# Performance work log

Measured on AMD Instinct MI355X. Metric: run time of the kernel, lower is better.

The kernel has to match this reference:

```python
import jax, jax.numpy as jnp
import numpy as np

B, S, T, E, H, V = 32, 64, 64, 512, 512, 32000  # batch, src len, tgt len, embed, hidden(per dir), vocab


def _lstm_scan(xs, Wih, Whh, bih, bhh, h0, c0):
    # xs: [S, B, E]; PyTorch gate order i, f, g, o
    def step(carry, x):
        h, c = carry
        g = x @ Wih.T + bih + h @ Whh.T + bhh
        i, f, gg, o = jnp.split(g, 4, axis=-1)
        c = jax.nn.sigmoid(f) * c + jax.nn.sigmoid(i) * jnp.tanh(gg)
        h = jax.nn.sigmoid(o) * jnp.tanh(c)
        return (h, c), h
    (hT, cT), hs = jax.lax.scan(step, (h0, c0), xs)
    return hs, hT, cT


def setup_inputs() -> dict:
    key = jax.random.key(0)
    ks = jax.random.split(key, 20)
    p = lambda k, shape, s=0.05: (jax.random.normal(k, shape, jnp.float32) * s)
    inp = {
        "input_chunk": jax.random.randint(ks[0], (B, S), 0, V),
        "target_chunk": jax.random.randint(ks[1], (B, T), 0, V),
        "enc_emb": jax.random.uniform(ks[2], (V, E), jnp.float32, -0.1, 0.1),
        "dec_emb": jax.random.uniform(ks[3], (V, E), jnp.float32, -0.1, 0.1),
        # encoder bidirectional LSTM (1 layer)
        "Wih_f": p(ks[4], (4 * H, E)), "Whh_f": p(ks[5], (4 * H, H)),
        "bih_f": p(ks[6], (4 * H,)), "bhh_f": p(ks[7], (4 * H,)),
        "Wih_b": p(ks[8], (4 * H, E)), "Whh_b": p(ks[9], (4 * H, H)),
        "bih_b": p(ks[10], (4 * H,)), "bhh_b": p(ks[11], (4 * H,)),
        # decoder LSTMCell: input 2H+E, hidden 2H
        "Wih_d": p(ks[12], (8 * H, 2 * H + E)), "Whh_d": p(ks[13], (8 * H, 2 * H)),
        "bih_d": p(ks[14], (8 * H,)), "bhh_d": p(ks[15], (8 * H,)),
        # attention projection 2H -> 2H
        "Wa": p(ks[16], (2 * H, 2 * H)), "ba": p(ks[17], (2 * H,)),
        # output projection 2H -> V (bias initialized to 0 in the module)
        "Wout": p(ks[18], (V, 2 * H)), "bout": jnp.zeros((V,), jnp.float32),
    }
    return inp


def reference(input_chunk, target_chunk, enc_emb, dec_emb,
              Wih_f, Whh_f, bih_f, bhh_f, Wih_b, Whh_b, bih_b, bhh_b,
              Wih_d, Whh_d, bih_d, bhh_d, Wa, ba, Wout, bout):
    # ---- Encoder: bidirectional LSTM ----
    x = enc_emb[input_chunk]                 # [B, S, E]
    xs = jnp.transpose(x, (1, 0, 2))         # [S, B, E]
    h0 = jnp.zeros((B, H), x.dtype)
    c0 = jnp.zeros((B, H), x.dtype)
    hs_f, hT_f, cT_f = _lstm_scan(xs, Wih_f, Whh_f, bih_f, bhh_f, h0, c0)
    hs_b, hT_b, cT_b = _lstm_scan(xs[::-1], Wih_b, Whh_b, bih_b, bhh_b, h0, c0)
    hs_b = hs_b[::-1]
    all_hidden = jnp.concatenate([hs_f, hs_b], axis=-1)          # [S, B, 2H]
    all_hidden = jnp.transpose(all_hidden, (1, 0, 2))            # [B, S, 2H]
    dec_h = jnp.concatenate([hT_f, hT_b], axis=-1)               # [B, 2H]
    dec_c = jnp.concatenate([cT_f, cT_b], axis=-1)               # [B, 2H]

    # ---- Decoder: attention + LSTMCell loop (teacher forcing = 1.0, no dropout) ----
    A = all_hidden @ Wa.T + ba               # W_attention(all_hidden), constant across steps
    tgt_emb = dec_emb[target_chunk]          # [B, T, E]
    # feed at t=0 is zeros; afterwards the t-th target embedding
    feeds = jnp.concatenate([jnp.zeros((B, 1, E), tgt_emb.dtype), tgt_emb[:, :-1]], axis=1)
    feeds = jnp.transpose(feeds, (1, 0, 2))  # [T, B, E]

    def dstep(carry, feed):
        h, c = carry
        scores = jnp.einsum('bsd,bd->bs', A, h)                  # [B, S]
        attn = jax.nn.softmax(scores, axis=1)
        ctx = jnp.einsum('bs,bsd->bd', attn, all_hidden)         # [B, 2H]
        inp = jnp.concatenate([ctx, feed], axis=1)               # [B, 2H+E]
        g = inp @ Wih_d.T + bih_d + h @ Whh_d.T + bhh_d
        i, f, gg, o = jnp.split(g, 4, axis=-1)
        c = jax.nn.sigmoid(f) * c + jax.nn.sigmoid(i) * jnp.tanh(gg)
        h = jax.nn.sigmoid(o) * jnp.tanh(c)
        logits = h @ Wout.T + bout                               # [B, V]
        return (h, c), logits

    _, logits = jax.lax.scan(dstep, (dec_h, dec_c), feeds)       # [T, B, V]
    logits = jnp.transpose(logits, (1, 0, 2))                    # [B, T, V]
    outputs = jnp.argmax(logits, axis=-1)                        # [B, T]
    return logits, outputs
```

## Files before the change

### kernel.cpp

```cpp
#include <hip/hip_runtime.h>
#include <hip/hip_bf16.h>

#define BB 32
#define SS 64
#define TT 64
#define EE 512
#define HH 512
#define VV 32000

#define O_C0    0u
#define O_C1    32768u
#define O_HD    65536u
#define O_CD    98304u
#define O_PENC  131072u
#define O_PDEC  655360u
#define O_CTX   1179648u
#define O_ALLH  1212416u
#define O_AATT  3309568u
#define O_HDEC  5406720u
#define O_PACK  7503872u
#define O_DA1   7507968u
#define O_DA2   7540736u
#define O_W1    7573504u
#define WS_NEED 95830016ull

#define S_GXF   0u
#define S_GXB   4194304u
#define S_GFEED 8388608u
#define U_BASE  17000000u

typedef float f32x4 __attribute__((ext_vector_type(4)));
typedef _Float16 f16x8 __attribute__((ext_vector_type(8)));
typedef _Float16 f16x4 __attribute__((ext_vector_type(4)));

__device__ __forceinline__ float sigm_(float x){ return 1.0f/(1.0f + expf(-x)); }

__device__ __forceinline__ unsigned int fkey_(float f){
  unsigned int u = __float_as_uint(f);
  return (u & 0x80000000u) ? ~u : (u | 0x80000000u);
}

__device__ __forceinline__ int swz_(int row, int kb){
  return (row*64 + kb) ^ ((row & 7) << 4);
}

__global__ __launch_bounds__(256) void k_init(float* __restrict__ ws){
  int i = blockIdx.x*256 + threadIdx.x;
  if (i < 65536) ws[i] = 0.0f;
  if (i < 2048) ((unsigned long long*)(ws + O_PACK))[i] = 0ull;
}

__global__ __launch_bounds__(256) void k_cvtW(
    const float* __restrict__ Whh_f, const float* __restrict__ Whh_b,
    const float* __restrict__ Wih_d, const float* __restrict__ Whh_d,
    _Float16* __restrict__ dst)
{
  int g = blockIdx.x*256 + threadIdx.x;
  int idx = g*4;
  f32x4 v;
  if (idx < 1048576){
    v = *(const f32x4*)(Whh_f + idx);
  } else if (idx < 2097152){
    v = *(const f32x4*)(Whh_b + (idx - 1048576));
  } else {
    int j = idx - 2097152;
    int row = j >> 11, col = j & 2047;
    const float* src = (col < 1024) ? (Wih_d + (size_t)row*1536 + col)
                                    : (Whh_d + (size_t)row*1024 + (col - 1024));
    v = *(const f32x4*)src;
  }
  f16x4 h;
  #pragma unroll
  for (int c = 0; c < 4; ++c) h[c] = (_Float16)v[c];
  *(f16x4*)(dst + idx) = h;
}

__global__ __launch_bounds__(256) void k_cvtWout(
    const float* __restrict__ Wout, _Float16* __restrict__ W1)
{
  size_t i = ((size_t)blockIdx.x*256 + threadIdx.x)*8;
  f32x4 x0 = *(const f32x4*)(Wout + i);
  f32x4 x1 = *(const f32x4*)(Wout + i + 4);
// ... 47 lines not shown
    Bs[(kq*4+3)*68 + lrow] = vw.w;
    __syncthreads();
    #pragma unroll
    for (int kk = 0; kk < 16; ++kk){
      float4 a4 = *(const float4*)&As[kk*68 + ty*4];
      float4 b4 = *(const float4*)&Bs[kk*68 + tx*4];
      float av[4] = {a4.x,a4.y,a4.z,a4.w};
      float bv[4] = {b4.x,b4.y,b4.z,b4.w};
      #pragma unroll
      for (int i=0;i<4;++i)
        #pragma unroll
        for (int j=0;j<4;++j)
          acc[i][j] = fmaf(av[i], bv[j], acc[i][j]);
    }
    __syncthreads();
  }
  float bv[4];
  #pragma unroll
  for (int j = 0; j < 4; ++j){
    int n = n0 + tx*4 + j;
    float bb = 0.f;
    if (bias0) bb += bias0[n];
    if (bias1) bb += bias1[n];
    bv[j] = bb;
  }
  #pragma unroll
  for (int i = 0; i < 4; ++i){
    int m = m0 + ty*4 + i;
    float4 v = make_float4(acc[i][0]+bv[0], acc[i][1]+bv[1], acc[i][2]+bv[2], acc[i][3]+bv[3]);
    *(float4*)&C[(size_t)m*ldC + n0 + tx*4] = v;
  }
}

__global__ __launch_bounds__(256) void k_enc_step(
    const _Float16* __restrict__ wenc,
    float* __restrict__ ws, const float* __restrict__ oscr, int t)
{
  __shared__ float hl[128*36];
  __shared__ float Wt[32*132];
  int sub = blockIdx.x, kp = blockIdx.y, dir = blockIdx.z;
  int tid = threadIdx.x;
  int s = dir ? (63 - t) : t;
  int p = t & 1;
  const float* gx  = oscr + (dir ? S_GXB : S_GXF);
  const float* prd = ws + (p ? O_PDEC : O_PENC) + dir*262144u;
  const float* cin = ws + O_C0 + p*32768u + dir*16384u;
  float* cout = ws + O_C0 + (p^1)*32768u + dir*16384u;

  {
    int ug = tid & 31, bg = tid >> 5;
    int ul0 = ug*4;
    int u0 = kp*128 + ul0;
    #pragma unroll
    for (int j = 0; j < 4; ++j){
      int b = bg*4 + j;
      size_t gbase = (size_t)(s*32 + b)*2048u;
      f32x4 g0 = *(const f32x4*)&gx[gbase + u0];
      f32x4 g1 = *(const f32x4*)&gx[gbase + 512 + u0];
      f32x4 g2 = *(const f32x4*)&gx[gbase + 1024 + u0];
      f32x4 g3 = *(const f32x4*)&gx[gbase + 1536 + u0];
      if (t > 0){
        #pragma unroll
        for (int kq = 0; kq < 4; ++kq){
          const float* pp = prd + kq*65536u + (size_t)b*2048u;
          g0 += *(const f32x4*)&pp[u0];
          g1 += *(const f32x4*)&pp[512 + u0];
          g2 += *(const f32x4*)&pp[1024 + u0];
          g3 += *(const f32x4*)&pp[1536 + u0];
        }
      }
      f32x4 c = *(const f32x4*)&cin[b*512 + u0];
      f32x4 cn, hn;
      #pragma unroll
      for (int e = 0; e < 4; ++e){
        float cc = sigm_(g1[e])*c[e] + sigm_(g0[e])*tanhf(g2[e]);
        float hh = sigm_(g3[e])*tanhf(cc);
        cn[e] = cc; hn[e] = hh;
        hl[(ul0+e)*36 + b] = hh;
      }
      if (sub == 0){
        *(f32x4*)&cout[b*512 + u0] = cn;
        *(f32x4*)&ws[O_ALLH + (size_t)(b*64 + s)*1024u + dir*512 + u0] = hn;
      }
    }
  }
  __syncthreads();
  if (t == 63) return;

  const _Float16* W = wenc + dir*1048576u;
  float* P = ws + (p ? O_PENC : O_PDEC) + dir*262144u + kp*65536u;
  int rg2 = tid & 31, bg2 = tid >> 5;
  int wrow = tid & 127, whalf = tid >> 7;
  float acc[4][4] = {};
  for (int kt = 0; kt < 4; ++kt){
    #pragma unroll
    for (int i = 0; i < 4; ++i){
      int chunk = whalf*4 + i;
      int grow = sub*128 + wrow;
      f16x4 v = *(const f16x4*)&W[(size_t)grow*512 + kp*128 + kt*32 + chunk*4];
      Wt[(chunk*4+0)*132 + wrow] = (float)v[0];
      Wt[(chunk*4+1)*132 + wrow] = (float)v[1];
      Wt[(chunk*4+2)*132 + wrow] = (float)v[2];
      Wt[(chunk*4+3)*132 + wrow] = (float)v[3];
    }
    __syncthreads();
    #pragma unroll 8
    for (int kk = 0; kk < 32; ++kk){
      f32x4 wv = *(const f32x4*)&Wt[kk*132 + rg2*4];
      f32x4 hv = *(const f32x4*)&hl[(kt*32+kk)*36 + bg2*4];
      #pragma unroll
      for (int i = 0; i < 4; ++i)
        #pragma unroll
        for (int j = 0; j < 4; ++j)
          acc[i][j] = fmaf(wv[i], hv[j], acc[i][j]);
    }
    __syncthreads();
  }
  #pragma unroll
  for (int j = 0; j < 4; ++j){
    int b = bg2*4 + j;
    f32x4 v; v[0]=acc[0][j]; v[1]=acc[1][j]; v[2]=acc[2][j]; v[3]=acc[3][j];
    *(f32x4*)&P[(size_t)b*2048u + sub*128 + rg2*4] = v;
  }
}

__global__ __launch_bounds__(256) void k_concat(float* __restrict__ ws){
  int i = blockIdx.x*256 + threadIdx.x;
  int which = i >> 15;
  int idx = i & 32767;
  int b = idx >> 10, u = idx & 1023;
  int dir = (u >= 512);
  int uu = u & 511;
  float v;
  if (which == 0){
    int s = dir ? 0 : 63;
    v = ws[O_ALLH + (size_t)(b*64 + s)*1024u + u];
  } else {
    v = ws[O_C0 + dir*16384u + b*512 + uu];
  }
  ws[(which ? O_CD : O_HD) + b*1024 + u] = v;
}

__global__ __launch_bounds__(256) void k_dec_gemm(
    const _Float16* __restrict__ wdec, float* __restrict__ ws)
{
  __shared__ char lds[16384];
  int nb = blockIdx.x, kp = blockIdx.y;
  int tid = threadIdx.x;
  int lane = tid & 63, w = tid >> 6;
  int lr = lane & 15, lg = lane >> 4;
  const _Float16* A1g = (const _Float16*)(ws + O_DA1);
  const _Float16* A2g = (const _Float16*)(ws + O_DA2);

  int aslot = tid & 127;
  int isA2  = tid >> 7;
  int arow = aslot >> 2, aseg = aslot & 3;
  int wrow = tid >> 2, wseg = tid & 3;
  const _Float16* asrc = (isA2 ? A2g : A1g) + (size_t)arow*2048u + kp*512 + aseg*8;
  const _Float16* wsrc = wdec + (size_t)(nb*64 + wrow)*2048u + kp*512 + wseg*8;

  f32x4 accH[2], accM[2];
  #pragma unroll
  for (int i = 0; i < 2; ++i){ f32x4 z; z[0]=z[1]=z[2]=z[3]=0.f; accH[i]=z; accM[i]=z; }

  uint4 rA, rW;
  rA = *(const uint4*)(asrc);
  rW = *(const uint4*)(wsrc);

  for (int kt = 0; kt < 16; ++kt){
    int cur = kt & 1;
    char* base = lds + cur*8192;
    *(uint4*)(base + (isA2 ? 2048 : 0) + swz_(arow, aseg*16)) = rA;
    *(uint4*)(base + 4096 + swz_(wrow, wseg*16)) = rW;
    __syncthreads();
    if (kt < 15){
      rA = *(const uint4*)(asrc + (kt+1)*32);
      rW = *(const uint4*)(wsrc + (kt+1)*32);
    }
    char* A1t = base, *A2t = base + 2048, *Wt = base + 4096;
    f16x8 wf = *(const f16x8*)(Wt + swz_(w*16 + lr, lg*16));
    #pragma unroll
    for (int mf = 0; mf < 2; ++mf){
      f16x8 a1 = *(const f16x8*)(A1t + swz_(mf*16 + lr, lg*16));
      f16x8 a2 = *(const f16x8*)(A2t + swz_(mf*16 + lr, lg*16));
      accH[mf] = __builtin_amdgcn_mfma_f32_16x16x32_f16(a1, wf, accH[mf], 0, 0, 0);
      accM[mf] = __builtin_amdgcn_mfma_f32_16x16x32_f16(a2, wf, accM[mf], 0, 0, 0);
    }
    __syncthreads();
  }
  const float rs = 1.0f/2048.0f;
  float* P = ws + O_PDEC + (size_t)kp*131072u;
  #pragma unroll
  for (int mf = 0; mf < 2; ++mf)
    #pragma unroll
    for (int r = 0; r < 4; ++r){
      int b = mf*16 + lg*4 + r;
      int n = nb*64 + w*16 + lr;
      P[(size_t)b*4096u + n] = accH[mf][r] + accM[mf][r]*rs;
    }
}

__global__ __launch_bounds__(256) void k_attn(float* __restrict__ ws,
                                              const float* __restrict__ oscr, int t){
  __shared__ float hlq[1024];
  __shared__ float part[64][5];
  __shared__ float sc[64];
  __shared__ float atn[64];
  __shared__ float dsh;
  int b = blockIdx.x, tid = threadIdx.x;
  float* hd = ws + O_HD;
  float* cd = ws + O_CD;
  _Float16* DA1 = (_Float16*)(ws + O_DA1);
  _Float16* DA2 = (_Float16*)(ws + O_DA2);
  if (t > 0){
    const float* gfd = oscr + S_GFEED + (size_t)((t-1)*32 + b)*4096u;
    const float* pd = ws + O_PDEC;
    for (int u = tid; u < 1024; u += 256){
      float g0 = gfd[u], g1 = gfd[1024+u], g2 = gfd[2048+u], g3 = gfd[3072+u];
      #pragma unroll
      for (int kp = 0; kp < 4; ++kp){
        const float* p = pd + (size_t)kp*131072u + (size_t)b*4096u;
        g0 += p[u]; g1 += p[1024+u]; g2 += p[2048+u]; g3 += p[3072+u];
      }
      float c = cd[b*1024 + u];
      c = sigm_(g1)*c + sigm_(g0)*tanhf(g2);
      float h = sigm_(g3)*tanhf(c);
      cd[b*1024+u] = c; hd[b*1024+u] = h; hlq[u] = h;
      ws[O_HDEC + (size_t)(b*64 + (t-1))*1024u + u] = h;
      _Float16 hi = (_Float16)h;
      DA1[(size_t)b*2048u + 1024 + u] = hi;
      DA2[(size_t)b*2048u + 1024 + u] = (_Float16)((h - (float)hi)*2048.0f);
    }
  } else {
    for (int u = tid; u < 1024; u += 256){
      float h = hd[b*1024 + u];
      hlq[u] = h;
      _Float16 hi = (_Float16)h;
      DA1[(size_t)b*2048u + 1024 + u] = hi;
      DA2[(size_t)b*2048u + 1024 + u] = (_Float16)((h - (float)hi)*2048.0f);
    }
  }
  __syncthreads();
  {
    int s = tid >> 2, p = tid & 3;
    const float* Ar = ws + O_AATT + (size_t)(b*64 + s)*1024u + p*256;
    const float* hp = &hlq[p*256];
    float sum = 0.f;
    #pragma unroll 8
    for (int k4 = 0; k4 < 64; ++k4){
      float4 a = *(const float4*)&Ar[k4*4];
      float4 h4 = *(const float4*)&hp[k4*4];
      sum = fmaf(a.x,h4.x, fmaf(a.y,h4.y, fmaf(a.z,h4.z, fmaf(a.w,h4.w, sum))));
    }
    part[s][p] = sum;
  }
  __syncthreads();
  if (tid < 64) sc[tid] = part[tid][0] + part[tid][1] + part[tid][2] + part[tid][3];
  __syncthreads();
  if (tid < 64){
    float m = sc[0];
    #pragma unroll
    for (int i = 1; i < 64; ++i) m = fmaxf(m, sc[i]);
    atn[tid] = expf(sc[tid] - m);
  }
  __syncthreads();
  if (tid == 0){
    float d = 0.f;
    #pragma unroll
    for (int i = 0; i < 64; ++i) d += atn[i];
    dsh = 1.0f/d;
  }
  __syncthreads();
  {
    float rd = dsh;
    float ax=0.f, ay=0.f, az=0.f, aw=0.f;
    const float* ah = ws + O_ALLH + (size_t)(b*64)*1024u + tid*4;
    for (int s2 = 0; s2 < 64; ++s2){
      float a = atn[s2];
      float4 v = *(const float4*)&ah[(size_t)s2*1024u];
      ax = fmaf(a, v.x, ax); ay = fmaf(a, v.y, ay);
      az = fmaf(a, v.z, az); aw = fmaf(a, v.w, aw);
    }
    float o[4] = {ax*rd, ay*rd, az*rd, aw*rd};
    #pragma unroll
    for (int j = 0; j < 4; ++j){
      int u = tid*4 + j;
      _Float16 hi = (_Float16)o[j];
      DA1[(size_t)b*2048u + u] = hi;
      DA2[(size_t)b*2048u + u] = (_Float16)((o[j] - (float)hi)*2048.0f);
    }
  }
}

__global__ __launch_bounds__(256) void k_dec_pw_last(float* __restrict__ ws,
                                                     const float* __restrict__ oscr){
  int g = blockIdx.x*256 + threadIdx.x;
  int b = g >> 10, u = g & 1023;
  const float* gfd = oscr + S_GFEED + (size_t)(63*32 + b)*4096u;
  const float* pd = ws + O_PDEC;
  float g0 = gfd[u], g1 = gfd[1024+u], g2 = gfd[2048+u], g3 = gfd[3072+u];
  #pragma unroll
  for (int kp = 0; kp < 4; ++kp){
    const float* p = pd + (size_t)kp*131072u + (size_t)b*4096u;
    g0 += p[u]; g1 += p[1024+u]; g2 += p[2048+u]; g3 += p[3072+u];
  }
  float c = ws[O_CD + b*1024 + u];
  c = sigm_(g1)*c + sigm_(g0)*tanhf(g2);
  float h = sigm_(g3)*tanhf(c);
  ws[O_HDEC + (size_t)(b*64 + 63)*1024u + u] = h;
}

__global__ __launch_bounds__(256) void k_cvtA(float* __restrict__ ws){
  const float* src = ws + O_HDEC;
  _Float16* A1 = (_Float16*)(ws + O_ALLH);
  _Float16* A2 = (_Float16*)(ws + O_AATT);
  int i = (blockIdx.x*256 + threadIdx.x)*8;
  f32x4 x0 = *(const f32x4*)&src[i];
  f32x4 x1 = *(const f32x4*)&src[i+4];
  f16x4 h0, h1, l0, l1;
  #pragma unroll
  for (int c = 0; c < 4; ++c){
    _Float16 a = (_Float16)x0[c];
    h0[c] = a; l0[c] = (_Float16)((x0[c] - (float)a)*2048.0f);
    _Float16 bq = (_Float16)x1[c];
    h1[c] = bq; l1[c] = (_Float16)((x1[c] - (float)bq)*2048.0f);
  }
  *(f16x4*)&A1[i]   = h0;
  *(f16x4*)&A1[i+4] = h1;
  *(f16x4*)&A2[i]   = l0;
  *(f16x4*)&A2[i+4] = l1;
}

__global__ __launch_bounds__(256) void k_logits(
    const _Float16* __restrict__ A1, const _Float16* __restrict__ A2,
    const _Float16* __restrict__ W1, const float* __restrict__ bout,
    float* __restrict__ out, unsigned long long* __restrict__ pk)
{
  __shared__ char lds[49152];
  int tid = threadIdx.x;
  int n0 = blockIdx.x*128, m0 = blockIdx.y*128;
  int lane = tid & 63, wave = tid >> 6;
  int wm = wave >> 1, wn = wave & 1;
  int lr = lane & 15, lg = lane >> 4;

  int s0 = tid*2, s1 = tid*2 + 1;
  int ar0 = s0 >> 2, as0 = s0 & 3;
  int ar1 = s1 >> 2, as1 = s1 & 3;
  const _Float16* a1p0 = A1 + (size_t)(m0 + ar0)*1024u + as0*8;
  const _Float16* a1p1 = A1 + (size_t)(m0 + ar1)*1024u + as1*8;
  const _Float16* a2p0 = A2 + (size_t)(m0 + ar0)*1024u + as0*8;
  const _Float16* a2p1 = A2 + (size_t)(m0 + ar1)*1024u + as1*8;
  const _Float16* wp0  = W1 + (size_t)(n0 + ar0)*1024u + as0*8;
  const _Float16* wp1  = W1 + (size_t)(n0 + ar1)*1024u + as1*8;

  f32x4 accH[4][4], accM[4][4];
  #pragma unroll
  for (int i = 0; i < 4; ++i)
    #pragma unroll
    for (int j = 0; j < 4; ++j){
      f32x4 z; z[0]=z[1]=z[2]=z[3]=0.f;
      accH[i][j] = z; accM[i][j] = z;
    }

  uint4 r10, r11, r20, r21, rw0, rw1;
  r10 = *(const uint4*)a1p0; r11 = *(const uint4*)a1p1;
  r20 = *(const uint4*)a2p0; r21 = *(const uint4*)a2p1;
  rw0 = *(const uint4*)wp0;  rw1 = *(const uint4*)wp1;

  for (int kt = 0; kt < 32; ++kt){
    int cur = kt & 1;
    char* base = lds + cur*24576;
    char* A1t = base, *A2t = base + 8192, *Wt = base + 16384;
    *(uint4*)(A1t + swz_(ar0, as0*16)) = r10;
// ... 184 lines not shown
  const float* enc_emb = (const float*)d_in[2];
  const float* dec_emb = (const float*)d_in[3];
  const float* Wih_f = (const float*)d_in[4];
  const float* Whh_f = (const float*)d_in[5];
  const float* bih_f = (const float*)d_in[6];
  const float* bhh_f = (const float*)d_in[7];
  const float* Wih_b = (const float*)d_in[8];
  const float* Whh_b = (const float*)d_in[9];
  const float* bih_b = (const float*)d_in[10];
  const float* bhh_b = (const float*)d_in[11];
  const float* Wih_d = (const float*)d_in[12];
  const float* Whh_d = (const float*)d_in[13];
  const float* bih_d = (const float*)d_in[14];
  const float* bhh_d = (const float*)d_in[15];
  const float* Wa   = (const float*)d_in[16];
  const float* ba   = (const float*)d_in[17];
  const float* Wout = (const float*)d_in[18];
  const float* bout = (const float*)d_in[19];
  float* ws = (float*)d_ws;
  float* out = (float*)d_out;
  float* oscr = (float*)d_out;
  _Float16* wf16 = (_Float16*)(oscr + U_BASE);
  bool bigws = (ws_size >= WS_NEED);

  k_init<<<256, 256, 0, stream>>>(ws);
  k_cvtW<<<10240, 256, 0, stream>>>(Whh_f, Whh_b, Wih_d, Whh_d, wf16);
  if (bigws)
    k_cvtWout<<<16000, 256, 0, stream>>>(Wout, (_Float16*)(ws + O_W1));

  k_gemm<1><<<dim3(32,32), 256, 0, stream>>>(enc_emb, 512, input_chunk, Wih_f, 512, bih_f, bhh_f, oscr + S_GXF, 2048, 512);
  k_gemm<1><<<dim3(32,32), 256, 0, stream>>>(enc_emb, 512, input_chunk, Wih_b, 512, bih_b, bhh_b, oscr + S_GXB, 2048, 512);
  k_gemm<2><<<dim3(64,32), 256, 0, stream>>>(dec_emb, 512, target_chunk, Wih_d + 1024, 1536, bih_d, bhh_d, oscr + S_GFEED, 4096, 512);

  for (int t = 0; t < 64; ++t){
    k_enc_step<<<dim3(16,4,2), 256, 0, stream>>>(wf16, ws, oscr, t);
  }

  k_concat<<<256, 256, 0, stream>>>(ws);
  k_gemm<0><<<dim3(16,32), 256, 0, stream>>>(ws + O_ALLH, 1024, nullptr, Wa, 1024, ba, nullptr, ws + O_AATT, 1024, 1024);

  const _Float16* wdec = wf16 + 2097152u;
  for (int t = 0; t < 64; ++t){
    k_attn<<<32, 256, 0, stream>>>(ws, oscr, t);
    k_dec_gemm<<<dim3(64,4), 256, 0, stream>>>(wdec, ws);
  }
  k_dec_pw_last<<<128, 256, 0, stream>>>(ws, oscr);

  k_cvtA<<<1024, 256, 0, stream>>>(ws);
  if (bigws){
    k_logits<<<dim3(250,16), 256, 0, stream>>>(
        (const _Float16*)(ws + O_ALLH), (const _Float16*)(ws + O_AATT),
        (const _Float16*)(ws + O_W1), bout, out, (unsigned long long*)(ws + O_PACK));
  } else {
    k_logits_fb<<<dim3(125,4), 512, 0, stream>>>(
        (const _Float16*)(ws + O_ALLH), (const _Float16*)(ws + O_AATT),
        Wout, bout, out, (unsigned long long*)(ws + O_PACK));
  }
  k_argmax<<<8, 256, 0, stream>>>((const unsigned long long*)(ws + O_PACK), out);
}
```

Baseline: 3.565 ms.

## Fuse per-step encoder and decoder launches into persistent kernels with grid barriers

Replaces the 64 per-timestep encoder launches and the 128 decoder attention/GEMM launches with two persistent kernels. Steps are synchronised by an atomic grid-wide barrier in workspace memory, and the concat, last-step pointwise and conversion kernels are folded in. The aim is to remove kernel launch overhead and inter-kernel gaps on the serial recurrence. The barrier assumes all blocks are co-resident and adds spin-wait cost per step. The logits grid is also reordered so that M tiles vary fastest.

```diff
diff --git a/kernel.cpp b/kernel.cpp
--- a/kernel.cpp
+++ b/kernel.cpp
@@ -44,10 +44,21 @@
   return (row*64 + kb) ^ ((row & 7) << 4);
 }
 
+__device__ __forceinline__ void gbar_(unsigned int* bar, unsigned int target){
+  __syncthreads();
+  if (threadIdx.x == 0){
+    __hip_atomic_fetch_add(bar, 1u, __ATOMIC_RELEASE, __HIP_MEMORY_SCOPE_AGENT);
+    while (__hip_atomic_load(bar, __ATOMIC_ACQUIRE, __HIP_MEMORY_SCOPE_AGENT) < target)
+      __builtin_amdgcn_s_sleep(2);
+  }
+  __syncthreads();
+}
+
 __global__ __launch_bounds__(256) void k_init(float* __restrict__ ws){
   int i = blockIdx.x*256 + threadIdx.x;
   if (i < 65536) ws[i] = 0.0f;
   if (i < 2048) ((unsigned long long*)(ws + O_PACK))[i] = 0ull;
+  if (i < 4) ((unsigned int*)(ws + O_CTX))[i] = 0u;
 }
 
 __global__ __launch_bounds__(256) void k_cvtW(
@@ -161,303 +172,318 @@
   }
 }
 
-__global__ __launch_bounds__(256) void k_enc_step(
+__global__ __launch_bounds__(256) void k_enc_all(
     const _Float16* __restrict__ wenc,
-    float* __restrict__ ws, const float* __restrict__ oscr, int t)
+    float* __restrict__ ws, const float* __restrict__ oscr)
 {
   __shared__ float hl[128*36];
   __shared__ float Wt[32*132];
-  int sub = blockIdx.x, kp = blockIdx.y, dir = blockIdx.z;
+  int bid = blockIdx.x;
+  int sub = bid & 15, kp = (bid >> 4) & 3, dir = bid >> 6;
   int tid = threadIdx.x;
-  int s = dir ? (63 - t) : t;
-  int p = t & 1;
-  const float* gx  = oscr + (dir ? S_GXB : S_GXF);
-  const float* prd = ws + (p ? O_PDEC : O_PENC) + dir*262144u;
-  const float* cin = ws + O_C0 + p*32768u + dir*16384u;
-  float* cout = ws + O_C0 + (p^1)*32768u + dir*16384u;
-
-  {
-    int ug = tid & 31, bg = tid >> 5;
-    int ul0 = ug*4;
-    int u0 = kp*128 + ul0;
+  unsigned int* bar = (unsigned int*)(ws + O_CTX);
+  const float* gx = oscr + (dir ? S_GXB : S_GXF);
+  const _Float16* W = wenc + dir*1048576u;
+
+  for (int t = 0; t < 64; ++t){
+    int s = dir ? (63 - t) : t;
+    int p = t & 1;
+    const float* prd = ws + (p ? O_PDEC : O_PENC) + dir*262144u;
+    const float* cin = ws + O_C0 + p*32768u + dir*16384u;
+    float* cout = ws + O_C0 + (p^1)*32768u + dir*16384u;
+
+    {
+      int ug = tid & 31, bg = tid >> 5;
+      int ul0 = ug*4;
+      int u0 = kp*128 + ul0;
+      #pragma unroll
+      for (int j = 0; j < 4; ++j){
+        int b = bg*4 + j;
+        size_t gbase = (size_t)(s*32 + b)*2048u;
+        f32x4 g0 = *(const f32x4*)&gx[gbase + u0];
+        f32x4 g1 = *(const f32x4*)&gx[gbase + 512 + u0];
+        f32x4 g2 = *(const f32x4*)&gx[gbase + 1024 + u0];
+        f32x4 g3 = *(const f32x4*)&gx[gbase + 1536 + u0];
+        if (t > 0){
+          #pragma unroll
+          for (int kq = 0; kq < 4; ++kq){
+            const float* pp = prd + kq*65536u + (size_t)b*2048u;
+            g0 += *(const f32x4*)&pp[u0];
+            g1 += *(const f32x4*)&pp[512 + u0];
+            g2 += *(const f32x4*)&pp[1024 + u0];
+            g3 += *(const f32x4*)&pp[1536 + u0];
+          }
+        }
+        f32x4 c = *(const f32x4*)&cin[b*512 + u0];
+        f32x4 cn, hn;
+        #pragma unroll
+        for (int e = 0; e < 4; ++e){
+          float cc = sigm_(g1[e])*c[e] + sigm_(g0[e])*tanhf(g2[e]);
+          float hh = sigm_(g3[e])*tanhf(cc);
+          cn[e] = cc; hn[e] = hh;
+          hl[(ul0+e)*36 + b] = hh;
+        }
+        if (sub == 0){
+          *(f32x4*)&cout[b*512 + u0] = cn;
+          *(f32x4*)&ws[O_ALLH + (size_t)(b*64 + s)*1024u + dir*512 + u0] = hn;
+        }
+      }
+    }
+    __syncthreads();
+    if (t == 63) break;
+
+    float* P = ws + (p ? O_PENC : O_PDEC) + dir*262144u + kp*65536u;
+    int rg2 = tid & 31, bg2 = tid >> 5;
+    int wrow = tid & 127, whalf = tid >> 7;
+    float acc[4][4] = {};
+    for (int kt = 0; kt < 4; ++kt){
+      #pragma unroll
+      for (int i = 0; i < 4; ++i){
+        int chunk = whalf*4 + i;
+        int grow = sub*128 + wrow;
+        f16x4 v = *(const f16x4*)&W[(size_t)grow*512 + kp*128 + kt*32 + chunk*4];
+        Wt[(chunk*4+0)*132 + wrow] = (float)v[0];
+        Wt[(chunk*4+1)*132 + wrow] = (float)v[1];
+        Wt[(chunk*4+2)*132 + wrow] = (float)v[2];
+        Wt[(chunk*4+3)*132 + wrow] = (float)v[3];
+      }
+      __syncthreads();
+      #pragma unroll 8
+      for (int kk = 0; kk < 32; ++kk){
+        f32x4 wv = *(const f32x4*)&Wt[kk*132 + rg2*4];
+        f32x4 hv = *(const f32x4*)&hl[(kt*32+kk)*36 + bg2*4];
+        #pragma unroll
+        for (int i = 0; i < 4; ++i)
+          #pragma unroll
+          for (int j = 0; j < 4; ++j)
+            acc[i][j] = fmaf(wv[i], hv[j], acc[i][j]);
+      }
+      __syncthreads();
+    }
     #pragma unroll
     for (int j = 0; j < 4; ++j){
-      int b = bg*4 + j;
-      size_t gbase = (size_t)(s*32 + b)*2048u;
-      f32x4 g0 = *(const f32x4*)&gx[gbase + u0];
-      f32x4 g1 = *(const f32x4*)&gx[gbase + 512 + u0];
-      f32x4 g2 = *(const f32x4*)&gx[gbase + 1024 + u0];
-      f32x4 g3 = *(const f32x4*)&gx[gbase + 1536 + u0];
-      if (t > 0){
-        #pragma unroll
-        for (int kq = 0; kq < 4; ++kq){
-          const float* pp = prd + kq*65536u + (size_t)b*2048u;
-          g0 += *(const f32x4*)&pp[u0];
-          g1 += *(const f32x4*)&pp[512 + u0];
-          g2 += *(const f32x4*)&pp[1024 + u0];
-          g3 += *(const f32x4*)&pp[1536 + u0];
-        }
-      }
-      f32x4 c = *(const f32x4*)&cin[b*512 + u0];
-      f32x4 cn, hn;
-      #pragma unroll
-      for (int e = 0; e < 4; ++e){
-        float cc = sigm_(g1[e])*c[e] + sigm_(g0[e])*tanhf(g2[e]);
-        float hh = sigm_(g3[e])*tanhf(cc);
-        cn[e] = cc; hn[e] = hh;
-        hl[(ul0+e)*36 + b] = hh;
-      }
-      if (sub == 0){
-        *(f32x4*)&cout[b*512 + u0] = cn;
-        *(f32x4*)&ws[O_ALLH + (size_t)(b*64 + s)*1024u + dir*512 + u0] = hn;
-      }
-    }
-  }
-  __syncthreads();
-  if (t == 63) return;
-
-  const _Float16* W = wenc + dir*1048576u;
-  float* P = ws + (p ? O_PENC : O_PDEC) + dir*262144u + kp*65536u;
-  int rg2 = tid & 31, bg2 = tid >> 5;
-  int wrow = tid & 127, whalf = tid >> 7;
-  float acc[4][4] = {};
-  for (int kt = 0; kt < 4; ++kt){
-    #pragma unroll
-    for (int i = 0; i < 4; ++i){
-      int chunk = whalf*4 + i;
-      int grow = sub*128 + wrow;
-      f16x4 v = *(const f16x4*)&W[(size_t)grow*512 + kp*128 + kt*32 + chunk*4];
-      Wt[(chunk*4+0)*132 + wrow] = (float)v[0];
-      Wt[(chunk*4+1)*132 + wrow] = (float)v[1];
-      Wt[(chunk*4+2)*132 + wrow] = (float)v[2];
-      Wt[(chunk*4+3)*132 + wrow] = (float)v[3];
-    }
-    __syncthreads();
-    #pragma unroll 8
-    for (int kk = 0; kk < 32; ++kk){
-      f32x4 wv = *(const f32x4*)&Wt[kk*132 + rg2*4];
-      f32x4 hv = *(const f32x4*)&hl[(kt*32+kk)*36 + bg2*4];
-      #pragma unroll
-      for (int i = 0; i < 4; ++i)
-        #pragma unroll
-        for (int j = 0; j < 4; ++j)
-          acc[i][j] = fmaf(wv[i], hv[j], acc[i][j]);
-    }
-    __syncthreads();
-  }
-  #pragma unroll
-  for (int j = 0; j < 4; ++j){
-    int b = bg2*4 + j;
-    f32x4 v; v[0]=acc[0][j]; v[1]=acc[1][j]; v[2]=acc[2][j]; v[3]=acc[3][j];
-    *(f32x4*)&P[(size_t)b*2048u + sub*128 + rg2*4] = v;
-  }
-}
-
-__global__ __launch_bounds__(256) void k_concat(float* __restrict__ ws){
-  int i = blockIdx.x*256 + threadIdx.x;
-  int which = i >> 15;
-  int idx = i & 32767;
-  int b = idx >> 10, u = idx & 1023;
-  int dir = (u >= 512);
-  int uu = u & 511;
-  float v;
-  if (which == 0){
-    int s = dir ? 0 : 63;
-    v = ws[O_ALLH + (size_t)(b*64 + s)*1024u + u];
-  } else {
-    v = ws[O_C0 + dir*16384u + b*512 + uu];
-  }
-  ws[(which ? O_CD : O_HD) + b*1024 + u] = v;
-}
-
-__global__ __launch_bounds__(256) void k_dec_gemm(
-    const _Float16* __restrict__ wdec, float* __restrict__ ws)
-{
-  __shared__ char lds[16384];
-  int nb = blockIdx.x, kp = blockIdx.y;
-  int tid = threadIdx.x;
-  int lane = tid & 63, w = tid >> 6;
-  int lr = lane & 15, lg = lane >> 4;
-  const _Float16* A1g = (const _Float16*)(ws + O_DA1);
-  const _Float16* A2g = (const _Float16*)(ws + O_DA2);
-
-  int aslot = tid & 127;
-  int isA2  = tid >> 7;
-  int arow = aslot >> 2, aseg = aslot & 3;
-  int wrow = tid >> 2, wseg = tid & 3;
-  const _Float16* asrc = (isA2 ? A2g : A1g) + (size_t)arow*2048u + kp*512 + aseg*8;
-  const _Float16* wsrc = wdec + (size_t)(nb*64 + wrow)*2048u + kp*512 + wseg*8;
-
-  f32x4 accH[2], accM[2];
-  #pragma unroll
-  for (int i = 0; i < 2; ++i){ f32x4 z; z[0]=z[1]=z[2]=z[3]=0.f; accH[i]=z; accM[i]=z; }
-
-  uint4 rA, rW;
-  rA = *(const uint4*)(asrc);
-  rW = *(const uint4*)(wsrc);
-
-  for (int kt = 0; kt < 16; ++kt){
-    int cur = kt & 1;
-    char* base = lds + cur*8192;
-    *(uint4*)(base + (isA2 ? 2048 : 0) + swz_(arow, aseg*16)) = rA;
-    *(uint4*)(base + 4096 + swz_(wrow, wseg*16)) = rW;
-    __syncthreads();
-    if (kt < 15){
-      rA = *(const uint4*)(asrc + (kt+1)*32);
-      rW = *(const uint4*)(wsrc + (kt+1)*32);
-    }
-    char* A1t = base, *A2t = base + 2048, *Wt = base + 4096;
-    f16x8 wf = *(const f16x8*)(Wt + swz_(w*16 + lr, lg*16));
-    #pragma unroll
-    for (int mf = 0; mf < 2; ++mf){
-      f16x8 a1 = *(const f16x8*)(A1t + swz_(mf*16 + lr, lg*16));
-      f16x8 a2 = *(const f16x8*)(A2t + swz_(mf*16 + lr, lg*16));
-      accH[mf] = __builtin_amdgcn_mfma_f32_16x16x32_f16(a1, wf, accH[mf], 0, 0, 0);
-      accM[mf] = __builtin_amdgcn_mfma_f32_16x16x32_f16(a2, wf, accM[mf], 0, 0, 0);
-    }
-    __syncthreads();
-  }
-  const float rs = 1.0f/2048.0f;
-  float* P = ws + O_PDEC + (size_t)kp*131072u;
-  #pragma unroll
-  for (int mf = 0; mf < 2; ++mf)
-    #pragma unroll
-    for (int r = 0; r < 4; ++r){
-      int b = mf*16 + lg*4 + r;
-      int n = nb*64 + w*16 + lr;
-      P[(size_t)b*4096u + n] = accH[mf][r] + accM[mf][r]*rs;
-    }
-}
-
-__global__ __launch_bounds__(256) void k_attn(float* __restrict__ ws,
-                                              const float* __restrict__ oscr, int t){
+      int b = bg2*4 + j;
+      f32x4 v; v[0]=acc[0][j]; v[1]=acc[1][j]; v[2]=acc[2][j]; v[3]=acc[3][j];
+      *(f32x4*)&P[(size_t)b*2048u + sub*128 + rg2*4] = v;
+    }
+    gbar_(bar, 128u*(unsigned)(t+1));
+  }
+}
+
+__global__ __launch_bounds__(256) void k_dec_all(
+    const _Float16* __restrict__ wdec,
+    float* __restrict__ ws, const float* __restrict__ oscr)
+{
   __shared__ float hlq[1024];
   __shared__ float part[64][5];
   __shared__ float sc[64];
   __shared__ float atn[64];
   __shared__ float dsh;
-  int b = blockIdx.x, tid = threadIdx.x;
+  __shared__ char glds[16384];
+  int bid = blockIdx.x, tid = threadIdx.x;
+  unsigned int* bar = ((unsigned int*)(ws + O_CTX)) + 1;
+  unsigned int bc = 0;
   float* hd = ws + O_HD;
   float* cd = ws + O_CD;
   _Float16* DA1 = (_Float16*)(ws + O_DA1);
   _Float16* DA2 = (_Float16*)(ws + O_DA2);
-  if (t > 0){
-    const float* gfd = oscr + S_GFEED + (size_t)((t-1)*32 + b)*4096u;
+  const float rs = 1.0f/2048.0f;
+
+  {
+    int i = bid*256 + tid;
+    int which = i >> 15, idx = i & 32767;
+    int b = idx >> 10, u = idx & 1023;
+    int dir = (u >= 512), uu = u & 511;
+    float v;
+    if (which == 0){
+      int s = dir ? 0 : 63;
+      v = ws[O_ALLH + (size_t)(b*64 + s)*1024u + u];
+    } else {
+      v = ws[O_C0 + dir*16384u + b*512 + uu];
+    }
+    ws[(which ? O_CD : O_HD) + b*1024 + u] = v;
+  }
+  gbar_(bar, 256u*(++bc));
+
+  for (int t = 0; t < 64; ++t){
+    if (bid < 32){
+      int b = bid;
+      if (t > 0){
+        const float* gfd = oscr + S_GFEED + (size_t)((t-1)*32 + b)*4096u;
+        const float* pd = ws + O_PDEC;
+        for (int u = tid; u < 1024; u += 256){
+          float g0 = gfd[u], g1 = gfd[1024+u], g2 = gfd[2048+u], g3 = gfd[3072+u];
+          #pragma unroll
+          for (int kp = 0; kp < 4; ++kp){
+            const float* p = pd + (size_t)kp*131072u + (size_t)b*4096u;
+            g0 += p[u]; g1 += p[1024+u]; g2 += p[2048+u]; g3 += p[3072+u];
+          }
+          float c = cd[b*1024 + u];
+          c = sigm_(g1)*c + sigm_(g0)*tanhf(g2);
+          float h = sigm_(g3)*tanhf(c);
+          cd[b*1024+u] = c; hd[b*1024+u] = h; hlq[u] = h;
+          ws[O_HDEC + (size_t)(b*64 + (t-1))*1024u + u] = h;
+          _Float16 hi = (_Float16)h;
+          DA1[(size_t)b*2048u + 1024 + u] = hi;
+          DA2[(size_t)b*2048u + 1024 + u] = (_Float16)((h - (float)hi)*2048.0f);
+        }
+      } else {
+        for (int u = tid; u < 1024; u += 256){
+          float h = hd[b*1024 + u];
+          hlq[u] = h;
+          _Float16 hi = (_Float16)h;
+          DA1[(size_t)b*2048u + 1024 + u] = hi;
+          DA2[(size_t)b*2048u + 1024 + u] = (_Float16)((h - (float)hi)*2048.0f);
+        }
+      }
+      __syncthreads();
+      {
+        int s = tid >> 2, p = tid & 3;
+        const float* Ar = ws + O_AATT + (size_t)(b*64 + s)*1024u + p*256;
+        const float* hp = &hlq[p*256];
+        float sum = 0.f;
+        #pragma unroll 8
+        for (int k4 = 0; k4 < 64; ++k4){
+          float4 a = *(const float4*)&Ar[k4*4];
+          float4 h4 = *(const float4*)&hp[k4*4];
+          sum = fmaf(a.x,h4.x, fmaf(a.y,h4.y, fmaf(a.z,h4.z, fmaf(a.w,h4.w, sum))));
+        }
+        part[s][p] = sum;
+      }
+      __syncthreads();
+      if (tid < 64) sc[tid] = part[tid][0] + part[tid][1] + part[tid][2] + part[tid][3];
+      __syncthreads();
+      if (tid < 64){
+        float m = sc[0];
+        #pragma unroll
+        for (int i = 1; i < 64; ++i) m = fmaxf(m, sc[i]);
+        atn[tid] = expf(sc[tid] - m);
+      }
+      __syncthreads();
+      if (tid == 0){
+        float d = 0.f;
+        #pragma unroll
+        for (int i = 0; i < 64; ++i) d += atn[i];
+        dsh = 1.0f/d;
+      }
+      __syncthreads();
+      {
+        float rd = dsh;
+        float ax=0.f, ay=0.f, az=0.f, aw=0.f;
+        const float* ah = ws + O_ALLH + (size_t)(b*64)*1024u + tid*4;
+        for (int s2 = 0; s2 < 64; ++s2){
+          float a = atn[s2];
+          float4 v = *(const float4*)&ah[(size_t)s2*1024u];
+          ax = fmaf(a, v.x, ax); ay = fmaf(a, v.y, ay);
+          az = fmaf(a, v.z, az); aw = fmaf(a, v.w, aw);
+        }
+        float o[4] = {ax*rd, ay*rd, az*rd, aw*rd};
+        #pragma unroll
+        for (int j = 0; j < 4; ++j){
+          int u = tid*4 + j;
+          _Float16 hi = (_Float16)o[j];
+          DA1[(size_t)b*2048u + u] = hi;
+          DA2[(size_t)b*2048u + u] = (_Float16)((o[j] - (float)hi)*2048.0f);
+        }
+      }
+    }
+    gbar_(bar, 256u*(++bc));
+
+    {
+      int nb = bid & 63, kp = bid >> 6;
+      int lane = tid & 63, w = tid >> 6;
+      int lr = lane & 15, lg = lane >> 4;
+      const _Float16* A1g = (const _Float16*)(ws + O_DA1);
+      const _Float16* A2g = (const _Float16*)(ws + O_DA2);
+      int aslot = tid & 127;
+      int isA2  = tid >> 7;
+      int arow = aslot >> 2, aseg = aslot & 3;
+      int wrow = tid >> 2, wseg = tid & 3;
+      const _Float16* asrc = (isA2 ? A2g : A1g) + (size_t)arow*2048u + kp*512 + aseg*8;
+      const _Float16* wsrc = wdec + (size_t)(nb*64 + wrow)*2048u + kp*512 + wseg*8;
+
+      f32x4 accH[2], accM[2];
+      #pragma unroll
+      for (int i = 0; i < 2; ++i){ f32x4 z; z[0]=z[1]=z[2]=z[3]=0.f; accH[i]=z; accM[i]=z; }
+
+      uint4 rA = *(const uint4*)(asrc);
+      uint4 rW = *(const uint4*)(wsrc);
+
+      for (int kt = 0; kt < 16; ++kt){
+        int cur = kt & 1;
+        char* base = glds + cur*8192;
+        *(uint4*)(base + (isA2 ? 2048 : 0) + swz_(arow, aseg*16)) = rA;
+        *(uint4*)(base + 4096 + swz_(wrow, wseg*16)) = rW;
+        __syncthreads();
+        if (kt < 15){
+          rA = *(const uint4*)(asrc + (kt+1)*32);
+          rW = *(const uint4*)(wsrc + (kt+1)*32);
+        }
+        char* A1t = base, *A2t = base + 2048, *Wt = base + 4096;
+        f16x8 wf = *(const f16x8*)(Wt + swz_(w*16 + lr, lg*16));
+        #pragma unroll
+        for (int mf = 0; mf < 2; ++mf){
+          f16x8 a1 = *(const f16x8*)(A1t + swz_(mf*16 + lr, lg*16));
+          f16x8 a2 = *(const f16x8*)(A2t + swz_(mf*16 + lr, lg*16));
+          accH[mf] = __builtin_amdgcn_mfma_f32_16x16x32_f16(a1, wf, accH[mf], 0, 0, 0);
+          accM[mf] = __builtin_amdgcn_mfma_f32_16x16x32_f16(a2, wf, accM[mf], 0, 0, 0);
+        }
+        __syncthreads();
+      }
+      float* P = ws + O_PDEC + (size_t)kp*131072u;
+      #pragma unroll
+      for (int mf = 0; mf < 2; ++mf)
+        #pragma unroll
+        for (int r = 0; r < 4; ++r){
+          int b = mf*16 + lg*4 + r;
+          int n = nb*64 + w*16 + lr;
+          P[(size_t)b*4096u + n] = accH[mf][r] + accM[mf][r]*rs;
+        }
+    }
+    gbar_(bar, 256u*(++bc));
+  }
+
+  if (bid < 128){
+    int g = bid*256 + tid;
+    int b = g >> 10, u = g & 1023;
+    const float* gfd = oscr + S_GFEED + (size_t)(63*32 + b)*4096u;
     const float* pd = ws + O_PDEC;
-    for (int u = tid; u < 1024; u += 256){
-      float g0 = gfd[u], g1 = gfd[1024+u], g2 = gfd[2048+u], g3 = gfd[3072+u];
-      #pragma unroll
-      for (int kp = 0; kp < 4; ++kp){
-        const float* p = pd + (size_t)kp*131072u + (size_t)b*4096u;
-        g0 += p[u]; g1 += p[1024+u]; g2 += p[2048+u]; g3 += p[3072+u];
-      }
-      float c = cd[b*1024 + u];
-      c = sigm_(g1)*c + sigm_(g0)*tanhf(g2);
-      float h = sigm_(g3)*tanhf(c);
-      cd[b*1024+u] = c; hd[b*1024+u] = h; hlq[u] = h;
-      ws[O_HDEC + (size_t)(b*64 + (t-1))*1024u + u] = h;
-      _Float16 hi = (_Float16)h;
-      DA1[(size_t)b*2048u + 1024 + u] = hi;
-      DA2[(size_t)b*2048u + 1024 + u] = (_Float16)((h - (float)hi)*2048.0f);
-    }
-  } else {
-    for (int u = tid; u < 1024; u += 256){
-      float h = hd[b*1024 + u];
-      hlq[u] = h;
-      _Float16 hi = (_Float16)h;
-      DA1[(size_t)b*2048u + 1024 + u] = hi;
-      DA2[(size_t)b*2048u + 1024 + u] = (_Float16)((h - (float)hi)*2048.0f);
-    }
-  }
-  __syncthreads();
+    float g0 = gfd[u], g1 = gfd[1024+u], g2 = gfd[2048+u], g3 = gfd[3072+u];
+    #pragma unroll
+    for (int kp = 0; kp < 4; ++kp){
+      const float* p = pd + (size_t)kp*131072u + (size_t)b*4096u;
+      g0 += p[u]; g1 += p[1024+u]; g2 += p[2048+u]; g3 += p[3072+u];
+    }
+    float c = ws[O_CD + b*1024 + u];
+    c = sigm_(g1)*c + sigm_(g0)*tanhf(g2);
+    float h = sigm_(g3)*tanhf(c);
+    ws[O_HDEC + (size_t)(b*64 + 63)*1024u + u] = h;
+  }
+  gbar_(bar, 256u*(++bc));
+
   {
-    int s = tid >> 2, p = tid & 3;
-    const float* Ar = ws + O_AATT + (size_t)(b*64 + s)*1024u + p*256;
-    const float* hp = &hlq[p*256];
-    float sum = 0.f;
-    #pragma unroll 8
-    for (int k4 = 0; k4 < 64; ++k4){
-      float4 a = *(const float4*)&Ar[k4*4];
-      float4 h4 = *(const float4*)&hp[k4*4];
-      sum = fmaf(a.x,h4.x, fmaf(a.y,h4.y, fmaf(a.z,h4.z, fmaf(a.w,h4.w, sum))));
-    }
-    part[s][p] = sum;
-  }
-  __syncthreads();
-  if (tid < 64) sc[tid] = part[tid][0] + part[tid][1] + part[tid][2] + part[tid][3];
-  __syncthreads();
-  if (tid < 64){
-    float m = sc[0];
-    #pragma unroll
-    for (int i = 1; i < 64; ++i) m = fmaxf(m, sc[i]);
-    atn[tid] = expf(sc[tid] - m);
-  }
-  __syncthreads();
-  if (tid == 0){
-    float d = 0.f;
-    #pragma unroll
-    for (int i = 0; i < 64; ++i) d += atn[i];
-    dsh = 1.0f/d;
-  }
-  __syncthreads();
-  {
-    float rd = dsh;
-    float ax=0.f, ay=0.f, az=0.f, aw=0.f;
-    const float* ah = ws + O_ALLH + (size_t)(b*64)*1024u + tid*4;
-    for (int s2 = 0; s2 < 64; ++s2){
-      float a = atn[s2];
-      float4 v = *(const float4*)&ah[(size_t)s2*1024u];
-      ax = fmaf(a, v.x, ax); ay = fmaf(a, v.y, ay);
-      az = fmaf(a, v.z, az); aw = fmaf(a, v.w, aw);
-    }
-    float o[4] = {ax*rd, ay*rd, az*rd, aw*rd};
-    #pragma unroll
-    for (int j = 0; j < 4; ++j){
-      int u = tid*4 + j;
-      _Float16 hi = (_Float16)o[j];
-      DA1[(size_t)b*2048u + u] = hi;
-      DA2[(size_t)b*2048u + u] = (_Float16)((o[j] - (float)hi)*2048.0f);
-    }
-  }
-}
-
-__global__ __launch_bounds__(256) void k_dec_pw_last(float* __restrict__ ws,
-                                                     const float* __restrict__ oscr){
-  int g = blockIdx.x*256 + threadIdx.x;
-  int b = g >> 10, u = g & 1023;
-  const float* gfd = oscr + S_GFEED + (size_t)(63*32 + b)*4096u;
-  const float* pd = ws + O_PDEC;
-  float g0 = gfd[u], g1 = gfd[1024+u], g2 = gfd[2048+u], g3 = gfd[3072+u];
-  #pragma unroll
-  for (int kp = 0; kp < 4; ++kp){
-    const float* p = pd + (size_t)kp*131072u + (size_t)b*4096u;
-    g0 += p[u]; g1 += p[1024+u]; g2 += p[2048+u]; g3 += p[3072+u];
-  }
-  float c = ws[O_CD + b*1024 + u];
-  c = sigm_(g1)*c + sigm_(g0)*tanhf(g2);
-  float h = sigm_(g3)*tanhf(c);
-  ws[O_HDEC + (size_t)(b*64 + 63)*1024u + u] = h;
-}
-
-__global__ __launch_bounds__(256) void k_cvtA(float* __restrict__ ws){
-  const float* src = ws + O_HDEC;
-  _Float16* A1 = (_Float16*)(ws + O_ALLH);
-  _Float16* A2 = (_Float16*)(ws + O_AATT);
-  int i = (blockIdx.x*256 + threadIdx.x)*8;
-  f32x4 x0 = *(const f32x4*)&src[i];
-  f32x4 x1 = *(const f32x4*)&src[i+4];
-  f16x4 h0, h1, l0, l1;
-  #pragma unroll
-  for (int c = 0; c < 4; ++c){
-    _Float16 a = (_Float16)x0[c];
-    h0[c] = a; l0[c] = (_Float16)((x0[c] - (float)a)*2048.0f);
-    _Float16 bq = (_Float16)x1[c];
-    h1[c] = bq; l1[c] = (_Float16)((x1[c] - (float)bq)*2048.0f);
-  }
-  *(f16x4*)&A1[i]   = h0;
-  *(f16x4*)&A1[i+4] = h1;
-  *(f16x4*)&A2[i]   = l0;
-  *(f16x4*)&A2[i+4] = l1;
+    const float* src = ws + O_HDEC;
+    _Float16* A1 = (_Float16*)(ws + O_ALLH);
+    _Float16* A2 = (_Float16*)(ws + O_AATT);
+    int g0 = bid*256 + tid;
+    for (int kq = 0; kq < 4; ++kq){
+      int i = (g0 + kq*65536)*8;
+      f32x4 x0 = *(const f32x4*)&src[i];
+      f32x4 x1 = *(const f32x4*)&src[i+4];
+      f16x4 h0, h1, l0, l1;
+      #pragma unroll
+      for (int c = 0; c < 4; ++c){
+        _Float16 a = (_Float16)x0[c];
+        h0[c] = a; l0[c] = (_Float16)((x0[c] - (float)a)*2048.0f);
+        _Float16 bq = (_Float16)x1[c];
+        h1[c] = bq; l1[c] = (_Float16)((x1[c] - (float)bq)*2048.0f);
+      }
+      *(f16x4*)&A1[i]   = h0;
+      *(f16x4*)&A1[i+4] = h1;
+      *(f16x4*)&A2[i]   = l0;
+      *(f16x4*)&A2[i+4] = l1;
+    }
+  }
 }
 
 __global__ __launch_bounds__(256) void k_logits(
@@ -467,7 +493,7 @@
 {
   __shared__ char lds[49152];
   int tid = threadIdx.x;
-  int n0 = blockIdx.x*128, m0 = blockIdx.y*128;
+  int n0 = blockIdx.y*128, m0 = blockIdx.x*128;
   int lane = tid & 63, wave = tid >> 6;
   int wm = wave >> 1, wn = wave & 1;
   int lr = lane & 15, lg = lane >> 4;
@@ -718,23 +744,15 @@
   k_gemm<1><<<dim3(32,32), 256, 0, stream>>>(enc_emb, 512, input_chunk, Wih_b, 512, bih_b, bhh_b, oscr + S_GXB, 2048, 512);
   k_gemm<2><<<dim3(64,32), 256, 0, stream>>>(dec_emb, 512, target_chunk, Wih_d + 1024, 1536, bih_d, bhh_d, oscr + S_GFEED, 4096, 512);
 
-  for (int t = 0; t < 64; ++t){
-    k_enc_step<<<dim3(16,4,2), 256, 0, stream>>>(wf16, ws, oscr, t);
-  }
-
-  k_concat<<<256, 256, 0, stream>>>(ws);
+  k_enc_all<<<128, 256, 0, stream>>>(wf16, ws, oscr);
+
   k_gemm<0><<<dim3(16,32), 256, 0, stream>>>(ws + O_ALLH, 1024, nullptr, Wa, 1024, ba, nullptr, ws + O_AATT, 1024, 1024);
 
   const _Float16* wdec = wf16 + 2097152u;
-  for (int t = 0; t < 64; ++t){
-    k_attn<<<32, 256, 0, stream>>>(ws, oscr, t);
-    k_dec_gemm<<<dim3(64,4), 256, 0, stream>>>(wdec, ws);
-  }
-  k_dec_pw_last<<<128, 256, 0, stream>>>(ws, oscr);
-
-  k_cvtA<<<1024, 256, 0, stream>>>(ws);
+  k_dec_all<<<256, 256, 0, stream>>>(wdec, ws, oscr);
+
   if (bigws){
-    k_logits<<<dim3(250,16), 256, 0, stream>>>(
+    k_logits<<<dim3(16,250), 256, 0, stream>>>(
         (const _Float16*)(ws + O_ALLH), (const _Float16*)(ws + O_AATT),
         (const _Float16*)(ws + O_W1), bout, out, (unsigned long long*)(ws + O_PACK));
   } else {
```

Result: slower. 10.05 ms (+181.9%).

## Drop split-K in decoder gate GEMM and reorder logits grid for weight reuse

Applied to the files above, without the earlier changes.

The per-step decoder gate GEMM no longer splits K four ways into partial buffers. It now uses 128 blocks that each cover 32 output columns over the full K=2048, writing the final gate preactivations directly. This removes the four-way partial sum reads in the attention and last pointwise kernels, but each block walks a longer K loop with fewer blocks in flight. The logits GEMM grid is also transposed so consecutive blocks share the same Wout tile across M, which should improve L2 reuse of the large weight matrix.

```diff
diff --git a/kernel.cpp b/kernel.cpp
--- a/kernel.cpp
+++ b/kernel.cpp
@@ -42,6 +42,9 @@
 
 __device__ __forceinline__ int swz_(int row, int kb){
   return (row*64 + kb) ^ ((row & 7) << 4);
+}
+__device__ __forceinline__ int swz128_(int row, int kb){
+  return (row*128 + kb) ^ ((row & 7) << 4);
 }
 
 __global__ __launch_bounds__(256) void k_init(float* __restrict__ ws){
@@ -270,65 +273,6 @@
   ws[(which ? O_CD : O_HD) + b*1024 + u] = v;
 }
 
-__global__ __launch_bounds__(256) void k_dec_gemm(
-    const _Float16* __restrict__ wdec, float* __restrict__ ws)
-{
-  __shared__ char lds[16384];
-  int nb = blockIdx.x, kp = blockIdx.y;
-  int tid = threadIdx.x;
-  int lane = tid & 63, w = tid >> 6;
-  int lr = lane & 15, lg = lane >> 4;
-  const _Float16* A1g = (const _Float16*)(ws + O_DA1);
-  const _Float16* A2g = (const _Float16*)(ws + O_DA2);
-
-  int aslot = tid & 127;
-  int isA2  = tid >> 7;
-  int arow = aslot >> 2, aseg = aslot & 3;
-  int wrow = tid >> 2, wseg = tid & 3;
-  const _Float16* asrc = (isA2 ? A2g : A1g) + (size_t)arow*2048u + kp*512 + aseg*8;
-  const _Float16* wsrc = wdec + (size_t)(nb*64 + wrow)*2048u + kp*512 + wseg*8;
-
-  f32x4 accH[2], accM[2];
-  #pragma unroll
-  for (int i = 0; i < 2; ++i){ f32x4 z; z[0]=z[1]=z[2]=z[3]=0.f; accH[i]=z; accM[i]=z; }
-
-  uint4 rA, rW;
-  rA = *(const uint4*)(asrc);
-  rW = *(const uint4*)(wsrc);
-
-  for (int kt = 0; kt < 16; ++kt){
-    int cur = kt & 1;
-    char* base = lds + cur*8192;
-    *(uint4*)(base + (isA2 ? 2048 : 0) + swz_(arow, aseg*16)) = rA;
-    *(uint4*)(base + 4096 + swz_(wrow, wseg*16)) = rW;
-    __syncthreads();
-    if (kt < 15){
-      rA = *(const uint4*)(asrc + (kt+1)*32);
-      rW = *(const uint4*)(wsrc + (kt+1)*32);
-    }
-    char* A1t = base, *A2t = base + 2048, *Wt = base + 4096;
-    f16x8 wf = *(const f16x8*)(Wt + swz_(w*16 + lr, lg*16));
-    #pragma unroll
-    for (int mf = 0; mf < 2; ++mf){
-      f16x8 a1 = *(const f16x8*)(A1t + swz_(mf*16 + lr, lg*16));
-      f16x8 a2 = *(const f16x8*)(A2t + swz_(mf*16 + lr, lg*16));
-      accH[mf] = __builtin_amdgcn_mfma_f32_16x16x32_f16(a1, wf, accH[mf], 0, 0, 0);
-      accM[mf] = __builtin_amdgcn_mfma_f32_16x16x32_f16(a2, wf, accM[mf], 0, 0, 0);
-    }
-    __syncthreads();
-  }
-  const float rs = 1.0f/2048.0f;
-  float* P = ws + O_PDEC + (size_t)kp*131072u;
-  #pragma unroll
-  for (int mf = 0; mf < 2; ++mf)
-    #pragma unroll
-    for (int r = 0; r < 4; ++r){
-      int b = mf*16 + lg*4 + r;
-      int n = nb*64 + w*16 + lr;
-      P[(size_t)b*4096u + n] = accH[mf][r] + accM[mf][r]*rs;
-    }
-}
-
 __global__ __launch_bounds__(256) void k_attn(float* __restrict__ ws,
                                               const float* __restrict__ oscr, int t){
   __shared__ float hlq[1024];
@@ -339,18 +283,16 @@
   int b = blockIdx.x, tid = threadIdx.x;
   float* hd = ws + O_HD;
   float* cd = ws + O_CD;
+  float* G  = ws + O_PDEC;
   _Float16* DA1 = (_Float16*)(ws + O_DA1);
   _Float16* DA2 = (_Float16*)(ws + O_DA2);
   if (t > 0){
     const float* gfd = oscr + S_GFEED + (size_t)((t-1)*32 + b)*4096u;
-    const float* pd = ws + O_PDEC;
     for (int u = tid; u < 1024; u += 256){
-      float g0 = gfd[u], g1 = gfd[1024+u], g2 = gfd[2048+u], g3 = gfd[3072+u];
-      #pragma unroll
-      for (int kp = 0; kp < 4; ++kp){
-        const float* p = pd + (size_t)kp*131072u + (size_t)b*4096u;
-        g0 += p[u]; g1 += p[1024+u]; g2 += p[2048+u]; g3 += p[3072+u];
-      }
+      float g0 = gfd[u]      + G[(size_t)b*4096u + u];
+      float g1 = gfd[1024+u] + G[(size_t)b*4096u + 1024 + u];
+      float g2 = gfd[2048+u] + G[(size_t)b*4096u + 2048 + u];
+      float g3 = gfd[3072+u] + G[(size_t)b*4096u + 3072 + u];
       float c = cd[b*1024 + u];
       c = sigm_(g1)*c + sigm_(g0)*tanhf(g2);
       float h = sigm_(g3)*tanhf(c);
@@ -421,18 +363,72 @@
   }
 }
 
+__global__ __launch_bounds__(256) void k_dec_gemm(
+    const _Float16* __restrict__ wdec, float* __restrict__ ws)
+{
+  __shared__ char glds[24576];
+  int bid = blockIdx.x, tid = threadIdx.x;
+  float* G = ws + O_PDEC;
+  const _Float16* DA1 = (const _Float16*)(ws + O_DA1);
+  const _Float16* DA2 = (const _Float16*)(ws + O_DA2);
+  const float rs = 1.0f/2048.0f;
+  int lane = tid & 63, w = tid >> 6;
+  int lr = lane & 15, lg = lane >> 4;
+  int mfw = w >> 1, nfw = w & 1;
+  int arow = tid >> 3, aseg = tid & 7;
+  const _Float16* a1src = DA1 + (size_t)arow*2048u + aseg*8;
+  const _Float16* a2src = DA2 + (size_t)arow*2048u + aseg*8;
+  const _Float16* wsrc  = wdec + (size_t)(bid*32 + arow)*2048u + aseg*8;
+  f32x4 accH, accM;
+  accH[0]=accH[1]=accH[2]=accH[3]=0.f;
+  accM[0]=accM[1]=accM[2]=accM[3]=0.f;
+  uint4 rA1 = *(const uint4*)a1src;
+  uint4 rA2 = *(const uint4*)a2src;
+  uint4 rW  = *(const uint4*)wsrc;
+  int so = swz128_(arow, aseg*16);
+  int raA = swz128_(mfw*16 + lr, lg*16);
+  int raW = swz128_(nfw*16 + lr, lg*16);
+  for (int kt = 0; kt < 32; ++kt){
+    char* base = glds + (kt & 1)*12288;
+    char* A1t = base; char* A2t = base + 4096; char* Wt = base + 8192;
+    *(uint4*)(A1t + so) = rA1;
+    *(uint4*)(A2t + so) = rA2;
+    *(uint4*)(Wt  + so) = rW;
+    __syncthreads();
+    if (kt < 31){
+      int ko = (kt+1)*64;
+      rA1 = *(const uint4*)(a1src + ko);
+      rA2 = *(const uint4*)(a2src + ko);
+      rW  = *(const uint4*)(wsrc + ko);
+    }
+    #pragma unroll
+    for (int ks = 0; ks < 2; ++ks){
+      f16x8 a1 = *(const f16x8*)(A1t + (raA ^ (ks*64)));
+      f16x8 a2 = *(const f16x8*)(A2t + (raA ^ (ks*64)));
+      f16x8 wf = *(const f16x8*)(Wt  + (raW ^ (ks*64)));
+      accH = __builtin_amdgcn_mfma_f32_16x16x32_f16(a1, wf, accH, 0, 0, 0);
+      accM = __builtin_amdgcn_mfma_f32_16x16x32_f16(a2, wf, accM, 0, 0, 0);
+    }
+    __syncthreads();
+  }
+  #pragma unroll
+  for (int r = 0; r < 4; ++r){
+    int b = mfw*16 + lg*4 + r;
+    int n = bid*32 + nfw*16 + lr;
+    G[(size_t)b*4096u + n] = accH[r] + accM[r]*rs;
+  }
+}
+
 __global__ __launch_bounds__(256) void k_dec_pw_last(float* __restrict__ ws,
                                                      const float* __restrict__ oscr){
   int g = blockIdx.x*256 + threadIdx.x;
   int b = g >> 10, u = g & 1023;
   const float* gfd = oscr + S_GFEED + (size_t)(63*32 + b)*4096u;
-  const float* pd = ws + O_PDEC;
-  float g0 = gfd[u], g1 = gfd[1024+u], g2 = gfd[2048+u], g3 = gfd[3072+u];
-  #pragma unroll
-  for (int kp = 0; kp < 4; ++kp){
-    const float* p = pd + (size_t)kp*131072u + (size_t)b*4096u;
-    g0 += p[u]; g1 += p[1024+u]; g2 += p[2048+u]; g3 += p[3072+u];
-  }
+  const float* G = ws + O_PDEC;
+  float g0 = gfd[u]      + G[(size_t)b*4096u + u];
+  float g1 = gfd[1024+u] + G[(size_t)b*4096u + 1024 + u];
+  float g2 = gfd[2048+u] + G[(size_t)b*4096u + 2048 + u];
+  float g3 = gfd[3072+u] + G[(size_t)b*4096u + 3072 + u];
   float c = ws[O_CD + b*1024 + u];
   c = sigm_(g1)*c + sigm_(g0)*tanhf(g2);
   float h = sigm_(g3)*tanhf(c);
@@ -467,7 +463,7 @@
 {
   __shared__ char lds[49152];
   int tid = threadIdx.x;
-  int n0 = blockIdx.x*128, m0 = blockIdx.y*128;
+  int n0 = blockIdx.y*128, m0 = blockIdx.x*128;
   int lane = tid & 63, wave = tid >> 6;
   int wm = wave >> 1, wn = wave & 1;
   int lr = lane & 15, lg = lane >> 4;
@@ -728,13 +724,13 @@
   const _Float16* wdec = wf16 + 2097152u;
   for (int t = 0; t < 64; ++t){
     k_attn<<<32, 256, 0, stream>>>(ws, oscr, t);
-    k_dec_gemm<<<dim3(64,4), 256, 0, stream>>>(wdec, ws);
+    k_dec_gemm<<<128, 256, 0, stream>>>(wdec, ws);
   }
   k_dec_pw_last<<<128, 256, 0, stream>>>(ws, oscr);
 
   k_cvtA<<<1024, 256, 0, stream>>>(ws);
   if (bigws){
-    k_logits<<<dim3(250,16), 256, 0, stream>>>(
+    k_logits<<<dim3(16,250), 256, 0, stream>>>(
         (const _Float16*)(ws + O_ALLH), (const _Float16*)(ws + O_AATT),
         (const _Float16*)(ws + O_W1), bout, out, (unsigned long long*)(ws + O_PACK));
   } else {
```

Result: slower. 4.064 ms (+14.0%).
